# Kernel tuning notes

Measured on AMD Instinct MI355X. Metric: run time of the kernel, lower is better.

Reference implementation:

```python
import jax, jax.numpy as jnp
import numpy as np

B, D, N, H = 1024, 512, 16, 512  # batch, latent, branches, hidden


def _lrelu(v):
    return jnp.where(v >= 0, v, 0.1 * v)  # LeakyReLU(0.1)


def setup_inputs() -> dict:
    key = jax.random.key(0)
    ks = jax.random.split(key, 9)
    s = 0.02
    return {
        "x": jax.random.normal(ks[0], (B, D, N), dtype=jnp.float32),
        "Ws1": jax.random.normal(ks[1], (D, D), dtype=jnp.float32) * s,
        "bs1": jnp.zeros((D,), dtype=jnp.float32),
        "Ws2": jax.random.normal(ks[2], (D, D), dtype=jnp.float32) * s,
        "bs2": jnp.zeros((D,), dtype=jnp.float32),
        # per-branch binary classifiers: Linear(D,H)+LeakyReLU+Linear(H,1)
        "Wc1": jax.random.normal(ks[3], (N, D, H), dtype=jnp.float32) * s,
        "bc1": jnp.zeros((N, H), dtype=jnp.float32),
        "Wc2": jax.random.normal(ks[4], (N, H), dtype=jnp.float32) * s,
        "bc2": jnp.zeros((N,), dtype=jnp.float32),
    }


def reference(x, Ws1, bs1, Ws2, bs2, Wc1, bc1, Wc2, bc2):
    # x: [B, D, N] -> per-branch tokens [B, N, D]
    xb = jnp.transpose(x, (0, 2, 1))
    # shared MLP applied to every branch slice (same weights)
    h = _lrelu(xb @ Ws1 + bs1)
    shared = _lrelu(h @ Ws2 + bs2)  # [B, N, D]
    # per-branch classifier on its own branch slice -> sigmoid probs
    h1 = _lrelu(jnp.einsum('bnd,ndh->bnh', shared, Wc1) + bc1)
    logits = jnp.einsum('bnh,nh->bn', h1, Wc2) + bc2  # [B, N]
    out = jax.nn.sigmoid(logits)[:, None, :]  # [B, 1, N]
    # full pass: concat branch slices along batch (branch-major), every
    # classifier applied to the full stack -> raw logits
    full_in = jnp.transpose(shared, (1, 0, 2)).reshape(N * B, D)  # [M, D]
    h2 = _lrelu(jnp.einsum('md,ndh->mnh', full_in, Wc1) + bc1)  # [M, N, H]
    full_logits = jnp.einsum('mnh,nh->mn', h2, Wc2) + bc2  # [M, N]
    full_out = full_logits[:, None, :]  # [N*B, 1, N]
    return (out, full_out)
```

## Files before the change

kernel.cpp:

```cpp
#include <hip/hip_runtime.h>
#include <hip/hip_bf16.h>
#include <stdint.h>

#define Bq 1024
#define Dq 512
#define Nq 16
#define Hq 512
#define Mq (Bq*Nq)

typedef short v8s __attribute__((ext_vector_type(8)));
typedef float v4f __attribute__((ext_vector_type(4)));
typedef int   v4i __attribute__((ext_vector_type(4)));

typedef __attribute__((address_space(3))) unsigned int as3_u32;
typedef __attribute__((address_space(1))) const unsigned int as1_u32;

__device__ __forceinline__ unsigned short f2bf(float f) {
  union { float f; unsigned u; } v; v.f = f;
  return (unsigned short)((v.u + 0x7fffu + ((v.u >> 16) & 1u)) >> 16);
}

__global__ void k_transpose_x(const float* __restrict__ x, unsigned short* __restrict__ xb) {
  __shared__ float lds[Dq][Nq + 1];
  const int b = blockIdx.x;
  const float* xi = x + (size_t)b * Dq * Nq;
  const int t = threadIdx.x;
  for (int p = 0; p < (Dq*Nq)/256; ++p) {
    int i = t + p*256;
    lds[i >> 4][i & (Nq-1)] = xi[i];
  }
  __syncthreads();
  unsigned short* o = xb + (size_t)b * Nq * Dq;
  for (int p = 0; p < (Dq*Nq)/256; ++p) {
    int i = t + p*256;
    o[i] = f2bf(lds[i & (Dq-1)][i >> 9]);
  }
}

__global__ void k_transpose_w(const float* __restrict__ Ws1, const float* __restrict__ Ws2,
                              const float* __restrict__ Wc1,
                              unsigned short* __restrict__ Ws1t, unsigned short* __restrict__ Ws2t,
                              unsigned short* __restrict__ Wc1t) {
  __shared__ float tile[32][33];
  const int z = blockIdx.z;
  const float* in;
  unsigned short* out;
  if (z == 0)      { in = Ws1; out = Ws1t; }
  else if (z == 1) { in = Ws2; out = Ws2t; }
  else             { in = Wc1 + (size_t)(z-2) * 512 * 512; out = Wc1t + (size_t)(z-2) * 512 * 512; }
  const int tx = threadIdx.x, ty = threadIdx.y;
  const int c0 = blockIdx.x * 32, r0 = blockIdx.y * 32;
#pragma unroll
  for (int j = 0; j < 4; ++j)
    tile[ty + j*8][tx] = in[(size_t)(r0 + ty + j*8) * 512 + c0 + tx];
  __syncthreads();
#pragma unroll
  for (int j = 0; j < 4; ++j) {
    int c = c0 + ty + j*8;
    int r = r0 + tx;
    out[(size_t)c * 512 + r] = f2bf(tile[tx][ty + j*8]);
  }
}

template<int MODE>
__global__ __launch_bounds__(256)
void k_gemm(const unsigned short* __restrict__ A,
            const unsigned short* __restrict__ Bt,
            const float* __restrict__ bias,
            void* __restrict__ out_,
            const float* __restrict__ w2,
            int permute) {
  constexpr int BM = 128, BN = 128, BK = 32, KD = 512;
  __shared__ __align__(16) unsigned short As[BM][BK];
  __shared__ __align__(16) unsigned short Bs[BN][BK];

  const int t = threadIdx.x;
  const int wave = t >> 6, lane = t & 63;
  const int wr = wave >> 1, wc = wave & 1;
  const int quad = lane >> 4, l16 = lane & 15;
  const int bm = blockIdx.x * BM, bn = blockIdx.y * BN;
  const int z = blockIdx.z;

  const unsigned short* Bz = Bt + (size_t)z * KD * 512;
  const float* biasz = bias + (size_t)z * 512;

  const int srow0 = wave * 32;
  const int lrow = lane >> 2;
  const int lslot = lane & 3;

  v4f acc[4][4] = {};

  for (int kt = 0; kt < KD / BK; ++kt) {
#pragma unroll
    for (int p = 0; p < 2; ++p) {
      int r0 = srow0 + p * 16;
      int row = r0 + lrow;
      int cg = lslot ^ ((row >> 1) & 3);
      const unsigned short* ga = &A [(size_t)(bm + row) * KD + kt*BK + cg*8];
      const unsigned short* gb = &Bz[(size_t)(bn + row) * KD + kt*BK + cg*8];
      __builtin_amdgcn_global_load_lds((as1_u32*)ga, (as3_u32*)&As[r0][0], 16, 0, 0);
      __builtin_amdgcn_global_load_lds((as1_u32*)gb, (as3_u32*)&Bs[r0][0], 16, 0, 0);
    }
    __syncthreads();
    v8s af[4], bf[4];
#pragma unroll
    for (int mi = 0; mi < 4; ++mi) {
      int ra = wr*64 + mi*16 + l16;
      af[mi] = *(const v8s*)&As[ra][(quad ^ ((ra >> 1) & 3)) * 8];
    }
#pragma unroll
    for (int ni = 0; ni < 4; ++ni) {
      int rb = wc*64 + ni*16 + l16;
      bf[ni] = *(const v8s*)&Bs[rb][(quad ^ ((rb >> 1) & 3)) * 8];
    }
#pragma unroll
    for (int mi = 0; mi < 4; ++mi)
#pragma unroll
      for (int ni = 0; ni < 4; ++ni)
        acc[mi][ni] = __builtin_amdgcn_mfma_f32_16x16x32_bf16(af[mi], bf[ni], acc[mi][ni], 0, 0, 0);
    __syncthreads();
  }

  if (MODE == 0) {
    unsigned short* O = (unsigned short*)out_;
#pragma unroll
    for (int mi = 0; mi < 4; ++mi) {
#pragma unroll
      for (int r = 0; r < 4; ++r) {
        int grow = bm + wr*64 + mi*16 + quad*4 + r;
        int orow = permute ? ((grow & 15) * Bq + (grow >> 4)) : grow;
#pragma unroll
        for (int ni = 0; ni < 4; ++ni) {
          int col = bn + wc*64 + ni*16 + l16;
          float v = acc[mi][ni][r] + biasz[col];
          v = v >= 0.f ? v : 0.1f * v;
          O[(size_t)orow * 512 + col] = f2bf(v);
        }
      }
    }
  } else {
    float* FL = (float*)out_;
    const float* w2z = w2 + (size_t)z * 512;
#pragma unroll
    for (int mi = 0; mi < 4; ++mi) {
#pragma unroll
      for (int r = 0; r < 4; ++r) {
        float s = 0.f;
#pragma unroll
        for (int ni = 0; ni < 4; ++ni) {
          int col = bn + wc*64 + ni*16 + l16;
          float v = acc[mi][ni][r] + biasz[col];
          v = v >= 0.f ? v : 0.1f * v;
          s += v * w2z[col];
        }
#pragma unroll
        for (int off = 1; off < 16; off <<= 1)
          s += __shfl_xor(s, off, 64);
        if (l16 == 0) {
          int grow = bm + wr*64 + mi*16 + quad*4 + r;
          atomicAdd(&FL[(size_t)grow * Nq + z], s);
        }
      }
    }
  }
}

__global__ void k_final(const float* __restrict__ fl, const float* __restrict__ bc2,
                        float* __restrict__ out) {
  int i = blockIdx.x * 256 + threadIdx.x;
  int m = i >> 4, n = i & 15;
  float v = fl[i] + bc2[n];
  out[Mq + i] = v;
  if (n == (m >> 10)) {
    int b = m & (Bq - 1);
    out[b * Nq + n] = 1.f / (1.f + __expf(-v));
  }
}

extern "C" void kernel_launch(void* const* d_in, const int* in_sizes, int n_in,
                              void* d_out, int out_size, void* d_ws, size_t ws_size,
                              hipStream_t stream) {
  (void)in_sizes; (void)n_in; (void)out_size; (void)ws_size;
  const float* x   = (const float*)d_in[0];
  const float* Ws1 = (const float*)d_in[1];
  const float* bs1 = (const float*)d_in[2];
  const float* Ws2 = (const float*)d_in[3];
  const float* bs2 = (const float*)d_in[4];
  const float* Wc1 = (const float*)d_in[5];
  const float* bc1 = (const float*)d_in[6];
  const float* Wc2 = (const float*)d_in[7];
  const float* bc2 = (const float*)d_in[8];

  char* ws = (char*)d_ws;
  unsigned short* Xb   = (unsigned short*)(ws);
  unsigned short* Hbuf = (unsigned short*)(ws + (size_t)16*1024*1024);
  unsigned short* Sm   = (unsigned short*)(ws + (size_t)32*1024*1024);
  unsigned short* Ws1t = (unsigned short*)(ws + (size_t)48*1024*1024);
  unsigned short* Ws2t = (unsigned short*)(ws + (size_t)48*1024*1024 + 512*1024);
  unsigned short* Wc1t = (unsigned short*)(ws + (size_t)49*1024*1024);
  float*          FL   = (float*)         (ws + (size_t)57*1024*1024);

  hipMemsetAsync(FL, 0, (size_t)Mq * Nq * sizeof(float), stream);

  k_transpose_x<<<Bq, 256, 0, stream>>>(x, Xb);
  k_transpose_w<<<dim3(16,16,18), dim3(32,8), 0, stream>>>(Ws1, Ws2, Wc1, Ws1t, Ws2t, Wc1t);

  k_gemm<0><<<dim3(128,4,1), 256, 0, stream>>>(Xb,   Ws1t, bs1, Hbuf, nullptr, 0);
  k_gemm<0><<<dim3(128,4,1), 256, 0, stream>>>(Hbuf, Ws2t, bs2, Sm,   nullptr, 1);
  k_gemm<1><<<dim3(128,4,16), 256, 0, stream>>>(Sm, Wc1t, bc1, FL, Wc2, 0);

  k_final<<<(Mq*Nq)/256, 256, 0, stream>>>(FL, bc2, (float*)d_out);
}
```

Measured before the change: 334.9 us.

## Switch GEMMs to 32x32x16 MFMA and use 256-row tiles for classifier GEMM

```diff
diff --git a/kernel.cpp b/kernel.cpp
--- a/kernel.cpp
+++ b/kernel.cpp
@@ -8,9 +8,9 @@
 #define Hq 512
 #define Mq (Bq*Nq)
 
-typedef short v8s __attribute__((ext_vector_type(8)));
-typedef float v4f __attribute__((ext_vector_type(4)));
-typedef int   v4i __attribute__((ext_vector_type(4)));
+typedef short v8s  __attribute__((ext_vector_type(8)));
+typedef float v16f __attribute__((ext_vector_type(16)));
+typedef int   v4i  __attribute__((ext_vector_type(4)));
 
 typedef __attribute__((address_space(3))) unsigned int as3_u32;
 typedef __attribute__((address_space(1))) const unsigned int as1_u32;
@@ -62,77 +62,92 @@
   }
 }
 
-template<int MODE>
-__global__ __launch_bounds__(256)
+template<int MODE, int BM>
+__global__ __launch_bounds__(256, 2)
 void k_gemm(const unsigned short* __restrict__ A,
             const unsigned short* __restrict__ Bt,
             const float* __restrict__ bias,
             void* __restrict__ out_,
             const float* __restrict__ w2,
             int permute) {
-  constexpr int BM = 128, BN = 128, BK = 32, KD = 512;
+  constexpr int BN = 128, BK = 32, KD = 512;
+  constexpr int NI = (BM == 256) ? 4 : 2;
+  constexpr int AG = BM / 16;
   __shared__ __align__(16) unsigned short As[BM][BK];
   __shared__ __align__(16) unsigned short Bs[BN][BK];
 
   const int t = threadIdx.x;
   const int wave = t >> 6, lane = t & 63;
-  const int wr = wave >> 1, wc = wave & 1;
-  const int quad = lane >> 4, l16 = lane & 15;
+  const int wr = (BM == 256) ? wave : (wave >> 1);
+  const int wc = (BM == 256) ? 0    : (wave & 1);
+  const int l32 = lane & 31, kh0 = lane >> 5;
   const int bm = blockIdx.x * BM, bn = blockIdx.y * BN;
   const int z = blockIdx.z;
 
   const unsigned short* Bz = Bt + (size_t)z * KD * 512;
   const float* biasz = bias + (size_t)z * 512;
 
-  const int srow0 = wave * 32;
   const int lrow = lane >> 2;
   const int lslot = lane & 3;
 
-  v4f acc[4][4] = {};
+  v16f acc[2][NI] = {};
 
   for (int kt = 0; kt < KD / BK; ++kt) {
 #pragma unroll
-    for (int p = 0; p < 2; ++p) {
-      int r0 = srow0 + p * 16;
-      int row = r0 + lrow;
-      int cg = lslot ^ ((row >> 1) & 3);
-      const unsigned short* ga = &A [(size_t)(bm + row) * KD + kt*BK + cg*8];
-      const unsigned short* gb = &Bz[(size_t)(bn + row) * KD + kt*BK + cg*8];
-      __builtin_amdgcn_global_load_lds((as1_u32*)ga, (as3_u32*)&As[r0][0], 16, 0, 0);
-      __builtin_amdgcn_global_load_lds((as1_u32*)gb, (as3_u32*)&Bs[r0][0], 16, 0, 0);
+    for (int i = wave; i < AG + 8; i += 4) {
+      const int isA = (i < AG);
+      const int r0 = (isA ? i : i - AG) * 16;
+      const int row = r0 + lrow;
+      const int cg = lslot ^ ((row >> 1) & 3);
+      const unsigned short* g = isA ? &A [(size_t)(bm + row) * KD + kt*BK + cg*8]
+                                    : &Bz[(size_t)(bn + row) * KD + kt*BK + cg*8];
+      as3_u32* d = isA ? (as3_u32*)&As[r0][0] : (as3_u32*)&Bs[r0][0];
+      __builtin_amdgcn_global_load_lds((as1_u32*)g, d, 16, 0, 0);
     }
     __syncthreads();
-    v8s af[4], bf[4];
-#pragma unroll
-    for (int mi = 0; mi < 4; ++mi) {
-      int ra = wr*64 + mi*16 + l16;
-      af[mi] = *(const v8s*)&As[ra][(quad ^ ((ra >> 1) & 3)) * 8];
-    }
-#pragma unroll
-    for (int ni = 0; ni < 4; ++ni) {
-      int rb = wc*64 + ni*16 + l16;
-      bf[ni] = *(const v8s*)&Bs[rb][(quad ^ ((rb >> 1) & 3)) * 8];
-    }
-#pragma unroll
-    for (int mi = 0; mi < 4; ++mi)
-#pragma unroll
-      for (int ni = 0; ni < 4; ++ni)
-        acc[mi][ni] = __builtin_amdgcn_mfma_f32_16x16x32_bf16(af[mi], bf[ni], acc[mi][ni], 0, 0, 0);
+    v8s af[2][2], bf[NI][2];
+#pragma unroll
+    for (int mi = 0; mi < 2; ++mi) {
+      int ra = wr*64 + mi*32 + l32;
+#pragma unroll
+      for (int kh = 0; kh < 2; ++kh) {
+        int c = kh*2 + kh0;
+        af[mi][kh] = *(const v8s*)&As[ra][(c ^ ((ra >> 1) & 3)) * 8];
+      }
+    }
+#pragma unroll
+    for (int ni = 0; ni < NI; ++ni) {
+      int rb = wc*64 + ni*32 + l32;
+#pragma unroll
+      for (int kh = 0; kh < 2; ++kh) {
+        int c = kh*2 + kh0;
+        bf[ni][kh] = *(const v8s*)&Bs[rb][(c ^ ((rb >> 1) & 3)) * 8];
+      }
+    }
+#pragma unroll
+    for (int kh = 0; kh < 2; ++kh)
+#pragma unroll
+      for (int mi = 0; mi < 2; ++mi)
+#pragma unroll
+        for (int ni = 0; ni < NI; ++ni)
+          acc[mi][ni] = __builtin_amdgcn_mfma_f32_32x32x16_bf16(af[mi][kh], bf[ni][kh], acc[mi][ni], 0, 0, 0);
     __syncthreads();
   }
 
   if (MODE == 0) {
     unsigned short* O = (unsigned short*)out_;
 #pragma unroll
-    for (int mi = 0; mi < 4; ++mi) {
-#pragma unroll
-      for (int r = 0; r < 4; ++r) {
-        int grow = bm + wr*64 + mi*16 + quad*4 + r;
-        int orow = permute ? ((grow & 15) * Bq + (grow >> 4)) : grow;
-#pragma unroll
-        for (int ni = 0; ni < 4; ++ni) {
-          int col = bn + wc*64 + ni*16 + l16;
-          float v = acc[mi][ni][r] + biasz[col];
+    for (int mi = 0; mi < 2; ++mi) {
+#pragma unroll
+      for (int ni = 0; ni < NI; ++ni) {
+        int col = bn + wc*64 + ni*32 + l32;
+        float bcol = biasz[col];
+#pragma unroll
+        for (int reg = 0; reg < 16; ++reg) {
+          int rl = (reg & 3) + 8*(reg >> 2) + 4*kh0;
+          int grow = bm + wr*64 + mi*32 + rl;
+          int orow = permute ? ((grow & 15) * Bq + (grow >> 4)) : grow;
+          float v = acc[mi][ni][reg] + bcol;
           v = v >= 0.f ? v : 0.1f * v;
           O[(size_t)orow * 512 + col] = f2bf(v);
         }
@@ -142,22 +157,23 @@
     float* FL = (float*)out_;
     const float* w2z = w2 + (size_t)z * 512;
 #pragma unroll
-    for (int mi = 0; mi < 4; ++mi) {
-#pragma unroll
-      for (int r = 0; r < 4; ++r) {
+    for (int mi = 0; mi < 2; ++mi) {
+#pragma unroll
+      for (int reg = 0; reg < 16; ++reg) {
+        int rl = (reg & 3) + 8*(reg >> 2) + 4*kh0;
         float s = 0.f;
 #pragma unroll
-        for (int ni = 0; ni < 4; ++ni) {
-          int col = bn + wc*64 + ni*16 + l16;
-          float v = acc[mi][ni][r] + biasz[col];
+        for (int ni = 0; ni < NI; ++ni) {
+          int col = bn + ni*32 + l32;
+          float v = acc[mi][ni][reg] + biasz[col];
           v = v >= 0.f ? v : 0.1f * v;
           s += v * w2z[col];
         }
 #pragma unroll
-        for (int off = 1; off < 16; off <<= 1)
+        for (int off = 1; off < 32; off <<= 1)
           s += __shfl_xor(s, off, 64);
-        if (l16 == 0) {
-          int grow = bm + wr*64 + mi*16 + quad*4 + r;
+        if (l32 == 0) {
+          int grow = bm + wave*64 + mi*32 + rl;
           atomicAdd(&FL[(size_t)grow * Nq + z], s);
         }
       }
@@ -205,9 +221,9 @@
   k_transpose_x<<<Bq, 256, 0, stream>>>(x, Xb);
   k_transpose_w<<<dim3(16,16,18), dim3(32,8), 0, stream>>>(Ws1, Ws2, Wc1, Ws1t, Ws2t, Wc1t);
 
-  k_gemm<0><<<dim3(128,4,1), 256, 0, stream>>>(Xb,   Ws1t, bs1, Hbuf, nullptr, 0);
-  k_gemm<0><<<dim3(128,4,1), 256, 0, stream>>>(Hbuf, Ws2t, bs2, Sm,   nullptr, 1);
-  k_gemm<1><<<dim3(128,4,16), 256, 0, stream>>>(Sm, Wc1t, bc1, FL, Wc2, 0);
+  k_gemm<0,128><<<dim3(128,4,1), 256, 0, stream>>>(Xb,   Ws1t, bs1, Hbuf, nullptr, 0);
+  k_gemm<0,128><<<dim3(128,4,1), 256, 0, stream>>>(Hbuf, Ws2t, bs2, Sm,   nullptr, 1);
+  k_gemm<1,256><<<dim3(64,4,16), 256, 0, stream>>>(Sm, Wc1t, bc1, FL, Wc2, 0);
 
   k_final<<<(Mq*Nq)/256, 256, 0, stream>>>(FL, bc2, (float*)d_out);
 }
```

After: 342.6 us. +2.3%, slower.
